# Performance work log

Hardware: AMD Instinct MI355X
Metric: run time of the kernel (lower is better)

Reference implementation:

```python
import jax, jax.numpy as jnp
import numpy as np

N_HEADS = 12
R = 0.5            # cfg.r kernel bandwidth
MASK_NEG = 10000.0


def _split_heads(t, n_heads):
    # (B, S, D) -> (B, H, S, W)
    B, S, D = t.shape
    return t.reshape(B, S, n_heads, D // n_heads).transpose(0, 2, 1, 3)


def setup_inputs() -> dict:
    key = jax.random.key(0)
    ks = jax.random.split(key, 8)
    B, S, D = 2, 256, 768
    sd = 1.0 / np.sqrt(D)
    x = jax.random.normal(ks[0], (B, S, D), dtype=jnp.float32)
    mask = jnp.ones((B, S), dtype=jnp.float32)
    Wq = jax.random.normal(ks[1], (D, D), dtype=jnp.float32) * sd
    bq = jnp.zeros((D,), dtype=jnp.float32)
    Wk = jax.random.normal(ks[2], (D, D), dtype=jnp.float32) * sd
    bk = jnp.zeros((D,), dtype=jnp.float32)
    Wv = jax.random.normal(ks[3], (D, D), dtype=jnp.float32) * sd
    bv = jnp.zeros((D,), dtype=jnp.float32)
    return {"x": x, "mask": mask, "Wq": Wq, "bq": bq, "Wk": Wk, "bk": bk, "Wv": Wv, "bv": bv}


def reference(x, mask, Wq, bq, Wk, bk, Wv, bv):
    B, S, D = x.shape
    H = N_HEADS
    # torch nn.Linear: y = x @ W.T + b
    q = _split_heads(x @ Wq.T + bq, H)   # (B, H, S, W)
    k = _split_heads(x @ Wk.T + bk, H)
    v = _split_heads(x @ Wv.T + bv, H)
    # sinc^4 product kernel over head width W: scores[b,h,l,i] = prod_w sinc(r*(q-k))^4
    diff = q[:, :, :, None, :] - k[:, :, None, :, :]          # (B, H, S, S, W)
    scores = jnp.prod(jnp.sinc(R * diff) ** 4, axis=-1)       # (B, H, S, S)
    scores = scores - MASK_NEG * (1.0 - mask[:, None, None, :])
    w = jax.nn.softmax(scores, axis=-1)                        # (B, H, S, S)
    y = w @ v                                                  # (B, H, S, W)
    y = y / w.sum(axis=-1, keepdims=True)                      # faithful (sums to 1)
    # merge heads: (B, H, S, W) -> (B, S, D)
    h = y.transpose(0, 2, 1, 3).reshape(B, S, D)
    return h
```

## Files before the change

kernel.cpp:

```cpp
#include <hip/hip_runtime.h>
#include <math.h>

#define NB 2
#define SS 256
#define DD 768
#define NH 12
#define WW 64

using f32x2  = __attribute__((ext_vector_type(2))) float;
using f32x4  = __attribute__((ext_vector_type(4))) float;
using bf16x8 = __attribute__((ext_vector_type(8))) short;

constexpr float R2  = 0.25f;
constexpr float C8  = 4.1168160e-7f;
constexpr float EPS = 1e-4f;
constexpr float THR = 0.0078125f;

#define QKV_ELEMS (NB*NH*SS*WW)
#define A_OFF_BYTES  4718592u
#define B_OFF_BYTES  6291456u
#define QT_OFF_BYTES 13369344u
#define KT_OFF_BYTES 18087936u

#define XBLKS 384
#define WBLKS 1728

__device__ __forceinline__ unsigned short bf16_rn(float f) {
    unsigned u = __builtin_bit_cast(unsigned, f);
    u += 0x7fffu + ((u >> 16) & 1u);
    return (unsigned short)(u >> 16);
}

__global__ __launch_bounds__(256) void conv_all(
        const float* __restrict__ x,
        const float* __restrict__ Wq, const float* __restrict__ Wk, const float* __restrict__ Wv,
        unsigned short* __restrict__ A, unsigned short* __restrict__ B) {
    int bid = blockIdx.x;
    const float* src;
    unsigned short* dstrow;
    if (bid < XBLKS) {
        int idx = bid * 256 + threadIdx.x;
        int m = idx / (DD/4);
        int c = (idx - m*(DD/4)) * 4;
        src = x + (size_t)idx * 4;
        dstrow = A + (size_t)m * 1536 + c;
    } else {
        int idx = (bid - XBLKS) * 256 + threadIdx.x;
        int p = idx / (768*192);
        int rem = idx - p*(768*192);
        const float* W = (p == 0) ? Wq : (p == 1) ? Wk : Wv;
        int j = rem / 192;
        int c = (rem - j*192) * 4;
        src = W + (size_t)rem * 4;
        dstrow = B + (size_t)(p*768 + j) * 1536 + c;
    }
    float4 v = *reinterpret_cast<const float4*>(src);
    float vv[4] = {v.x, v.y, v.z, v.w};
    unsigned short h[4], l[4];
    #pragma unroll
    for (int e = 0; e < 4; ++e) {
        h[e] = bf16_rn(vv[e]);
        float hf = __builtin_bit_cast(float, (unsigned)h[e] << 16);
        l[e] = bf16_rn(vv[e] - hf);
    }
    *reinterpret_cast<ushort4*>(dstrow)       = make_ushort4(h[0], h[1], h[2], h[3]);
    *reinterpret_cast<ushort4*>(dstrow + 768) = make_ushort4(l[0], l[1], l[2], l[3]);
}

__global__ __launch_bounds__(256, 2) void gemm_qkv(
        const unsigned short* __restrict__ A, const unsigned short* __restrict__ B,
        const float* __restrict__ bq, const float* __restrict__ bk, const float* __restrict__ bv,
        float* __restrict__ qkv, float* __restrict__ QT, float* __restrict__ KT) {
    __shared__ float red[4][32*32];
    const int tid = threadIdx.x;
    const int wid = tid >> 6, l = tid & 63;
    const int lr = l & 15, lo_ = l >> 4;
    const int m0 = blockIdx.x * 32, n0 = blockIdx.y * 32;

    const unsigned short* Ap = A + (size_t)(m0 + lr) * 1536 + wid * 192 + lo_ * 8;
    const unsigned short* Bp = B + (size_t)(n0 + lr) * 1536 + wid * 192 + lo_ * 8;

    f32x4 acc00 = 0.f, acc01 = 0.f, acc10 = 0.f, acc11 = 0.f;

    bf16x8 a0[3], a1[3], b0[3], b1[3];
    #define LDSTEP(s, bi) { \
        const int seg_ = (s)/6, kq_ = (s) - seg_*6; \
        const int ao_ = ((seg_ == 2) ? 768 : 0) + kq_*32; \
        const int bo_ = ((seg_ == 1) ? 768 : 0) + kq_*32; \
        a0[bi] = *reinterpret_cast<const bf16x8*>(Ap + ao_); \
        a1[bi] = *reinterpret_cast<const bf16x8*>(Ap + 16*1536 + ao_); \
        b0[bi] = *reinterpret_cast<const bf16x8*>(Bp + bo_); \
        b1[bi] = *reinterpret_cast<const bf16x8*>(Bp + 16*1536 + bo_); }

    LDSTEP(0, 0)
    LDSTEP(1, 1)
    #pragma unroll
    for (int it = 0; it < 18; ++it) {
        if (it + 2 < 18) { LDSTEP(it + 2, (it + 2) % 3) }
        const int cb = it % 3;
        acc00 = __builtin_amdgcn_mfma_f32_16x16x32_bf16(a0[cb], b0[cb], acc00, 0, 0, 0);
        acc01 = __builtin_amdgcn_mfma_f32_16x16x32_bf16(a0[cb], b1[cb], acc01, 0, 0, 0);
        acc10 = __builtin_amdgcn_mfma_f32_16x16x32_bf16(a1[cb], b0[cb], acc10, 0, 0, 0);
        acc11 = __builtin_amdgcn_mfma_f32_16x16x32_bf16(a1[cb], b1[cb], acc11, 0, 0, 0);
    }
    #undef LDSTEP

    #pragma unroll
    for (int j = 0; j < 4; ++j) {
        int r0 = lo_ * 4 + j;
        red[wid][(r0     ) * 32 + lr     ] = acc00[j];
        red[wid][(r0     ) * 32 + lr + 16] = acc01[j];
        red[wid][(r0 + 16) * 32 + lr     ] = acc10[j];
        red[wid][(r0 + 16) * 32 + lr + 16] = acc11[j];
    }
    __syncthreads();

    int row = tid >> 3, col = (tid & 7) * 4;
    f32x4 s = *reinterpret_cast<f32x4*>(&red[0][row*32 + col]);
    #pragma unroll
    for (int w = 1; w < 4; ++w)
        s += *reinterpret_cast<f32x4*>(&red[w][row*32 + col]);

    int n = n0 + col;
    int which = n / 768;
    int jj = n - which * 768;
    const float* bias = (which == 0) ? bq : (which == 1) ? bk : bv;
    float4 bb = *reinterpret_cast<const float4*>(&bias[jj]);
    s[0] += bb.x; s[1] += bb.y; s[2] += bb.z; s[3] += bb.w;

    int m = m0 + row, b_ = m >> 8, s_ = m & 255;
    int head = jj >> 6, w = jj & 63;
    int bh = b_ * NH + head;

    if (which == 2) {
        float* o = qkv + (size_t)2 * QKV_ELEMS + ((size_t)bh * SS + s_) * WW + w;
        *reinterpret_cast<float4*>(o) = make_float4(s[0], s[1], s[2], s[3]);
    } else if (which == 0) {
        float* qtb = QT + ((size_t)bh * SS + s_) * 192 + w;
        f32x4 av, sv, cv;
        #pragma unroll
        for (int e = 0; e < 4; ++e) {
            float a = R2 * s[e];
            av[e] = a;
            sv[e] = __builtin_amdgcn_sinf(a);
            cv[e] = __builtin_amdgcn_cosf(a);
        }
        *reinterpret_cast<f32x4*>(qtb)       = av;
        *reinterpret_cast<f32x4*>(qtb + 64)  = sv;
        *reinterpret_cast<f32x4*>(qtb + 128) = cv;
    } else {
        float* ktb = KT + (size_t)bh * WW * 3 * SS;
        #pragma unroll
        for (int e = 0; e < 4; ++e) {
            int d = w + e;
            float a = R2 * s[e];
            ktb[(d*3 + 0) * SS + s_] = a;
            ktb[(d*3 + 1) * SS + s_] = __builtin_amdgcn_sinf(a);
            ktb[(d*3 + 2) * SS + s_] = __builtin_amdgcn_cosf(a);
        }
    }
}

__global__ __launch_bounds__(256, 3) void fattn(
    const float* __restrict__ qkv, const float* __restrict__ QT, const float* __restrict__ KT,
    const float* __restrict__ mask, float* __restrict__ out)
{
    const int bh = blockIdx.y;
    const int b = bh / NH, h = bh - b * NH;
    const int row0 = blockIdx.x * 8;

    const float* Vg = qkv + (size_t)(2 * QKV_ELEMS) + (size_t)bh * SS * WW;
    const float* kt = KT + (size_t)bh * WW * 3 * SS;
    const float* qb = QT + ((size_t)bh * SS + row0) * 192;

    __shared__ __align__(16) float ebuf[SS][8];
    __shared__ __align__(16) float ypart[4][8][WW];
    __shared__ float zs[4][8];

    const int tid = threadIdx.x, lane = tid & 63, wid = tid >> 6;
    const float mt = -10000.0f * (1.0f - mask[b * SS + tid]);

    float pg[8] = {1.f,1.f,1.f,1.f,1.f,1.f,1.f,1.f};

    auto score_group = [&](int g) {
        const float* kg = kt + (size_t)g * 24 * SS + tid;
        float kk[8], sk[8], ck[8];
        #pragma unroll
        for (int j = 0; j < 8; ++j) {
            kk[j] = kg[j * 3 * SS];
            sk[j] = kg[j * 3 * SS + SS];
            ck[j] = kg[j * 3 * SS + 2 * SS];
        }
        #pragma unroll
        for (int r = 0; r < 8; ++r) {
            const float* qr = qb + r * 192 + g * 8;
            float4 q0 = *reinterpret_cast<const float4*>(qr);
            float4 q1 = *reinterpret_cast<const float4*>(qr + 4);
            float4 s0 = *reinterpret_cast<const float4*>(qr + 64);
            float4 s1 = *reinterpret_cast<const float4*>(qr + 68);
            float4 c0 = *reinterpret_cast<const float4*>(qr + 128);
            float4 c1 = *reinterpret_cast<const float4*>(qr + 132);
            float qa[8] = {q0.x,q0.y,q0.z,q0.w,q1.x,q1.y,q1.z,q1.w};
            float sa[8] = {s0.x,s0.y,s0.z,s0.w,s1.x,s1.y,s1.z,s1.w};
            float ca[8] = {c0.x,c0.y,c0.z,c0.w,c1.x,c1.y,c1.z,c1.w};
            float ps = 1.f, pt = 1.f;
            #pragma unroll
            for (int j = 0; j < 8; ++j) {
                float t  = qa[j] - kk[j];
                float at = fmaxf(fabsf(t), EPS);
                float sn = fmaf(sa[j], ck[j], -(ca[j] * sk[j]));
                sn = (fabsf(t) < EPS) ? at : sn;
                ps *= sn;
                pt *= at;
            }
            pg[r] *= (ps * C8) * __builtin_amdgcn_rcpf(pt);
        }
    };

    for (int g = 0; g < 3; ++g) score_group(g);

    bool alive[8];
    bool any8 = false;
    #pragma unroll
    for (int r = 0; r < 8; ++r) {
        alive[r] = __any(fabsf(pg[r]) > THR);
        any8 = any8 || alive[r];
    }
    if (any8) {
        #pragma unroll 1
        for (int g = 3; g < 8; ++g) {
            const float* kg = kt + (size_t)g * 24 * SS + tid;
            float kk[8], sk[8], ck[8];
            #pragma unroll
            for (int j = 0; j < 8; ++j) {
                kk[j] = kg[j * 3 * SS];
                sk[j] = kg[j * 3 * SS + SS];
                ck[j] = kg[j * 3 * SS + 2 * SS];
            }
            bool still = false;
            #pragma unroll
            for (int r = 0; r < 8; ++r) {
                if (alive[r]) {
                    const float* qr = qb + r * 192 + g * 8;
                    float4 q0 = *reinterpret_cast<const float4*>(qr);
                    float4 q1 = *reinterpret_cast<const float4*>(qr + 4);
                    float4 s0 = *reinterpret_cast<const float4*>(qr + 64);
                    float4 s1 = *reinterpret_cast<const float4*>(qr + 68);
                    float4 c0 = *reinterpret_cast<const float4*>(qr + 128);
                    float4 c1 = *reinterpret_cast<const float4*>(qr + 132);
                    float qa[8] = {q0.x,q0.y,q0.z,q0.w,q1.x,q1.y,q1.z,q1.w};
                    float sa[8] = {s0.x,s0.y,s0.z,s0.w,s1.x,s1.y,s1.z,s1.w};
                    float ca[8] = {c0.x,c0.y,c0.z,c0.w,c1.x,c1.y,c1.z,c1.w};
                    float ps = 1.f, pt = 1.f;
                    #pragma unroll
                    for (int j = 0; j < 8; ++j) {
                        float t  = qa[j] - kk[j];
                        float at = fmaxf(fabsf(t), EPS);
                        float sn = fmaf(sa[j], ck[j], -(ca[j] * sk[j]));
                        sn = (fabsf(t) < EPS) ? at : sn;
                        ps *= sn;
                        pt *= at;
                    }
                    pg[r] *= (ps * C8) * __builtin_amdgcn_rcpf(pt);
                    alive[r] = __any(fabsf(pg[r]) > THR);
                }
                still = still || alive[r];
            }
            if (!still) break;
        }
    }

    float e[8];
    #pragma unroll
    for (int r = 0; r < 8; ++r) {
        float p = pg[r];
        p *= p; p *= p;
        e[r] = __expf(p + mt);
    }
    {
        f32x4 e0, e1;
        #pragma unroll
        for (int r = 0; r < 4; ++r) { e0[r] = e[r]; e1[r] = e[r+4]; }
        *reinterpret_cast<f32x4*>(&ebuf[tid][0]) = e0;
        *reinterpret_cast<f32x4*>(&ebuf[tid][4]) = e1;
    }
    #pragma unroll
    for (int r = 0; r < 8; ++r) {
        float z = e[r];
        #pragma unroll
        for (int off = 32; off; off >>= 1) z += __shfl_xor(z, off);
        if (lane == 0) zs[wid][r] = z;
    }

    f32x2 y01 = {0.f,0.f}, y23 = {0.f,0.f}, y45 = {0.f,0.f}, y67 = {0.f,0.f};
    const float* vb = Vg + (size_t)(wid * 64) * WW + lane;
    #pragma unroll 16
    for (int ii = 0; ii < 64; ++ii) {
        float v = vb[ii * WW];
        f32x2 vv; vv[0] = v; vv[1] = v;
        f32x4 ea = *reinterpret_cast<const f32x4*>(&ebuf[wid*64 + ii][0]);
        f32x4 eb = *reinterpret_cast<const f32x4*>(&ebuf[wid*64 + ii][4]);
        f32x2 e01; e01[0] = ea[0]; e01[1] = ea[1];
        f32x2 e23; e23[0] = ea[2]; e23[1] = ea[3];
        f32x2 e45; e45[0] = eb[0]; e45[1] = eb[1];
        f32x2 e67; e67[0] = eb[2]; e67[1] = eb[3];
        y01 += e01 * vv;
        y23 += e23 * vv;
        y45 += e45 * vv;
        y67 += e67 * vv;
    }
    ypart[wid][0][lane] = y01[0]; ypart[wid][1][lane] = y01[1];
    ypart[wid][2][lane] = y23[0]; ypart[wid][3][lane] = y23[1];
    ypart[wid][4][lane] = y45[0]; ypart[wid][5][lane] = y45[1];
    ypart[wid][6][lane] = y67[0]; ypart[wid][7][lane] = y67[1];
    __syncthreads();

    {
        const int r0 = tid >> 6;
        #pragma unroll
        for (int q = 0; q < 2; ++q) {
            int rr = r0 + q * 4;
            float yy = ypart[0][rr][lane] + ypart[1][rr][lane]
                     + ypart[2][rr][lane] + ypart[3][rr][lane];
            float zz = zs[0][rr] + zs[1][rr] + zs[2][rr] + zs[3][rr];
            out[((size_t)b * SS + row0 + rr) * DD + h * WW + lane] = yy * __builtin_amdgcn_rcpf(zz);
        }
    }
}

extern "C" void kernel_launch(void* const* d_in, const int* in_sizes, int n_in,
                              void* d_out, int out_size, void* d_ws, size_t ws_size,
                              hipStream_t stream) {
    const float* x    = (const float*)d_in[0];
    const float* mask = (const float*)d_in[1];
    const float* Wq   = (const float*)d_in[2];
    const float* bq   = (const float*)d_in[3];
    const float* Wk   = (const float*)d_in[4];
    const float* bk   = (const float*)d_in[5];
    const float* Wv   = (const float*)d_in[6];
    const float* bv   = (const float*)d_in[7];
    float* out = (float*)d_out;

    float*          qkv = (float*)d_ws;
    unsigned short* Ab  = (unsigned short*)((char*)d_ws + A_OFF_BYTES);
    unsigned short* Bb  = (unsigned short*)((char*)d_ws + B_OFF_BYTES);
    float*          QTp = (float*)((char*)d_ws + QT_OFF_BYTES);
    float*          KTp = (float*)((char*)d_ws + KT_OFF_BYTES);

    conv_all<<<dim3(XBLKS + WBLKS), 256, 0, stream>>>(x, Wq, Wk, Wv, Ab, Bb);
    gemm_qkv<<<dim3(512/32, 2304/32), 256, 0, stream>>>(Ab, Bb, bq, bk, bv, qkv, QTp, KTp);
    fattn<<<dim3(SS/8, NB*NH), 256, 0, stream>>>(qkv, QTp, KTp, mask, out);
}
```

Measured before the change: 57.08 us.

## Remap block indices to XCDs for cache locality and double-buffer K loads

Both the QKV GEMM and the attention kernel now launch a 1D grid and decode block indices so that blocks landing on the same XCD (round-robin by bid&7) share the same weight columns or the same batch-head. The intent is for each XCD's private L2 to serve repeated reads of B tiles and K/V data instead of spreading them across all XCDs. The attention kernel also double-buffers the per-group K/sin/cos register loads in the first three groups so the next group's global loads are issued before the current group's math. The extra register buffers may raise register pressure at launch bound 3.

```diff
diff --git a/kernel.cpp b/kernel.cpp
--- a/kernel.cpp
+++ b/kernel.cpp
@@ -75,7 +75,12 @@
     const int tid = threadIdx.x;
     const int wid = tid >> 6, l = tid & 63;
     const int lr = l & 15, lo_ = l >> 4;
-    const int m0 = blockIdx.x * 32, n0 = blockIdx.y * 32;
+
+    const int bid = blockIdx.x;
+    const int xcd = bid & 7, idx = bid >> 3;
+    const int n_t = xcd * 9 + (idx >> 4);
+    const int m_t = idx & 15;
+    const int m0 = m_t * 32, n0 = n_t * 32;
 
     const unsigned short* Ap = A + (size_t)(m0 + lr) * 1536 + wid * 192 + lo_ * 8;
     const unsigned short* Bp = B + (size_t)(n0 + lr) * 1536 + wid * 192 + lo_ * 8;
@@ -165,9 +170,12 @@
     const float* __restrict__ qkv, const float* __restrict__ QT, const float* __restrict__ KT,
     const float* __restrict__ mask, float* __restrict__ out)
 {
-    const int bh = blockIdx.y;
+    const int bid = blockIdx.x;
+    const int xcd = bid & 7, idx = bid >> 3;
+    const int bh = xcd * 3 + (idx >> 5);
+    const int row0 = (idx & 31) * 8;
+
     const int b = bh / NH, h = bh - b * NH;
-    const int row0 = blockIdx.x * 8;
 
     const float* Vg = qkv + (size_t)(2 * QKV_ELEMS) + (size_t)bh * SS * WW;
     const float* kt = KT + (size_t)bh * WW * 3 * SS;
@@ -182,15 +190,14 @@
 
     float pg[8] = {1.f,1.f,1.f,1.f,1.f,1.f,1.f,1.f};
 
-    auto score_group = [&](int g) {
-        const float* kg = kt + (size_t)g * 24 * SS + tid;
-        float kk[8], sk[8], ck[8];
-        #pragma unroll
-        for (int j = 0; j < 8; ++j) {
-            kk[j] = kg[j * 3 * SS];
-            sk[j] = kg[j * 3 * SS + SS];
-            ck[j] = kg[j * 3 * SS + 2 * SS];
-        }
+    float kk[2][8], sk[2][8], ck[2][8];
+    #define LOADK(g, bi) { const float* kg_ = kt + (size_t)(g) * 24 * SS + tid; \
+        _Pragma("unroll") for (int j = 0; j < 8; ++j) { \
+            kk[bi][j] = kg_[j * 3 * SS]; \
+            sk[bi][j] = kg_[j * 3 * SS + SS]; \
+            ck[bi][j] = kg_[j * 3 * SS + 2 * SS]; } }
+
+    auto score_buf = [&](int g, int bi) {
         #pragma unroll
         for (int r = 0; r < 8; ++r) {
             const float* qr = qb + r * 192 + g * 8;
@@ -206,9 +213,9 @@
             float ps = 1.f, pt = 1.f;
             #pragma unroll
             for (int j = 0; j < 8; ++j) {
-                float t  = qa[j] - kk[j];
+                float t  = qa[j] - kk[bi][j];
                 float at = fmaxf(fabsf(t), EPS);
-                float sn = fmaf(sa[j], ck[j], -(ca[j] * sk[j]));
+                float sn = fmaf(sa[j], ck[bi][j], -(ca[j] * sk[bi][j]));
                 sn = (fabsf(t) < EPS) ? at : sn;
                 ps *= sn;
                 pt *= at;
@@ -217,7 +224,12 @@
         }
     };
 
-    for (int g = 0; g < 3; ++g) score_group(g);
+    LOADK(0, 0)
+    LOADK(1, 1)
+    score_buf(0, 0);
+    LOADK(2, 0)
+    score_buf(1, 1);
+    score_buf(2, 0);
 
     bool alive[8];
     bool any8 = false;
@@ -229,14 +241,7 @@
     if (any8) {
         #pragma unroll 1
         for (int g = 3; g < 8; ++g) {
-            const float* kg = kt + (size_t)g * 24 * SS + tid;
-            float kk[8], sk[8], ck[8];
-            #pragma unroll
-            for (int j = 0; j < 8; ++j) {
-                kk[j] = kg[j * 3 * SS];
-                sk[j] = kg[j * 3 * SS + SS];
-                ck[j] = kg[j * 3 * SS + 2 * SS];
-            }
+            LOADK(g, 0)
             bool still = false;
             #pragma unroll
             for (int r = 0; r < 8; ++r) {
@@ -254,9 +259,9 @@
                     float ps = 1.f, pt = 1.f;
                     #pragma unroll
                     for (int j = 0; j < 8; ++j) {
-                        float t  = qa[j] - kk[j];
+                        float t  = qa[j] - kk[0][j];
                         float at = fmaxf(fabsf(t), EPS);
-                        float sn = fmaf(sa[j], ck[j], -(ca[j] * sk[j]));
+                        float sn = fmaf(sa[j], ck[0][j], -(ca[j] * sk[0][j]));
                         sn = (fabsf(t) < EPS) ? at : sn;
                         ps *= sn;
                         pt *= at;
@@ -269,6 +274,7 @@
             if (!still) break;
         }
     }
+    #undef LOADK
 
     float e[8];
     #pragma unroll
@@ -348,6 +354,6 @@
     float*          KTp = (float*)((char*)d_ws + KT_OFF_BYTES);
 
     conv_all<<<dim3(XBLKS + WBLKS), 256, 0, stream>>>(x, Wq, Wk, Wv, Ab, Bb);
-    gemm_qkv<<<dim3(512/32, 2304/32), 256, 0, stream>>>(Ab, Bb, bq, bk, bv, qkv, QTp, KTp);
-    fattn<<<dim3(SS/8, NB*NH), 256, 0, stream>>>(qkv, QTp, KTp, mask, out);
-}
+    gemm_qkv<<<dim3(1152), 256, 0, stream>>>(Ab, Bb, bq, bk, bv, qkv, QTp, KTp);
+    fattn<<<dim3(768), 256, 0, stream>>>(qkv, QTp, KTp, mask, out);
+}
```

Result: slower. 72.33 us (+26.7%).
